# Performance work log

Hardware: AMD Instinct MI355X
Metric: run time of the kernel (lower is better)

Reference implementation:

```python
import jax, jax.numpy as jnp
import numpy as np

N, E, G = 10000, 80000, 32
Z, C, B, H = 10, 128, 8, 64
R_MAX = 5.0
AVG_NEIGH = 16.0
L_OFF = [0, 1, 4, 9, 16]  # slice offsets for l = 0..3 blocks of the SH vector


def real_sh(u):
    # Real spherical harmonics up to l=3, 'component' normalization (sum_m Y_lm^2 = 2l+1)
    x, y, z = u[:, 0], u[:, 1], u[:, 2]
    s3, s5, s15 = 3.0 ** 0.5, 5.0 ** 0.5, 15.0 ** 0.5
    cols = [
        jnp.ones_like(x),
        s3 * x, s3 * y, s3 * z,
        s15 * x * y, s15 * y * z, (s5 / 2) * (3 * z ** 2 - 1),
        s15 * x * z, (s15 / 2) * (x ** 2 - y ** 2),
        (70.0 ** 0.5 / 4) * (3 * x ** 2 * y - y ** 3),
        105.0 ** 0.5 * x * y * z,
        (42.0 ** 0.5 / 4) * y * (5 * z ** 2 - 1),
        (7.0 ** 0.5 / 2) * (5 * z ** 3 - 3 * z),
        (42.0 ** 0.5 / 4) * x * (5 * z ** 2 - 1),
        (105.0 ** 0.5 / 2) * z * (x ** 2 - y ** 2),
        (70.0 ** 0.5 / 4) * (x ** 3 - 3 * x * y ** 2),
    ]
    return jnp.stack(cols, axis=-1)  # [E, 16]


def poly_cutoff(x, p=5):
    f = (1.0 - (p + 1) * (p + 2) / 2 * x ** p
         + p * (p + 2) * x ** (p + 1)
         - p * (p + 1) / 2 * x ** (p + 2))
    return f * (x < 1.0).astype(f.dtype)


def setup_inputs() -> dict:
    key = jax.random.key(0)
    ks = jax.random.split(key, 20)
    vectors = jax.random.normal(ks[0], (E, 3), dtype=jnp.float32) * 1.5
    elem = jax.random.randint(ks[1], (N,), 0, Z)
    node_attrs = jax.nn.one_hot(elem, Z, dtype=jnp.float32)
    edge_index = jax.random.randint(ks[2], (2, E), 0, N).astype(jnp.int64)
    batch = jnp.sort(jax.random.randint(ks[3], (N,), 0, G)).astype(jnp.int64)

    def init(k, shape, fan_in):
        return jax.random.normal(k, shape, dtype=jnp.float32) / np.sqrt(fan_in)

    return {
        "vectors": vectors,
        "node_attrs": node_attrs,
        "W_embed": init(ks[4], (Z, C), Z),
        "atomic_energies": -jnp.arange(1, Z + 1, dtype=jnp.float32),
        "rw1": init(ks[5], (2, B, H), B),
        "rw2": init(ks[6], (2, H, H), H),
        "rw3": init(ks[7], (2, H, H), H),
        "rw4": init(ks[8], (2, H, 4 * C), H),
        "Wmix": init(ks[9], (2, 4, C, C), C),
        "U": init(ks[10], (2, Z, 4), Z),
        "Wprod": init(ks[11], (2, C, C), C),
        "Wsc": init(ks[12], (2, C, C), C),
        "Wro0": init(ks[13], (C, 1), C),
        "Wro1a": init(ks[14], (C, 16), C),
        "Wro1b": init(ks[15], (16, 1), 16),
        "scale": jnp.array([1.0], dtype=jnp.float32),
        "shift": jnp.array([0.0], dtype=jnp.float32),
        "edge_index": edge_index,
        "batch": batch,
    }


def reference(vectors, node_attrs, W_embed, atomic_energies, rw1, rw2, rw3, rw4,
              Wmix, U, Wprod, Wsc, Wro0, Wro1a, Wro1b, scale, shift,
              edge_index, batch):
    sender, receiver = edge_index[0], edge_index[1]
    r = jnp.linalg.norm(vectors, axis=-1)                     # [E]
    u = vectors / r[:, None]
    Y = real_sh(u)                                            # [E, 16]
    n = jnp.arange(1, B + 1, dtype=vectors.dtype)
    bessel = jnp.sqrt(2.0 / R_MAX) * jnp.sin(n[None] * jnp.pi * r[:, None] / R_MAX) / r[:, None]
    edge_feats = bessel * poly_cutoff(r / R_MAX)[:, None]     # [E, B]

    h = node_attrs @ W_embed                                  # [N, C] node embedding
    node_e0 = node_attrs @ atomic_energies                    # [N] atomic reference energies
    e0 = jax.ops.segment_sum(node_e0, batch, num_segments=G)  # [G]

    node_inter = jnp.zeros((node_attrs.shape[0],), dtype=vectors.dtype)
    for i in range(2):  # interaction layers (fixed small count)
        f = jax.nn.silu(edge_feats @ rw1[i])
        f = jax.nn.silu(f @ rw2[i])
        f = jax.nn.silu(f @ rw3[i])
        R_w = (f @ rw4[i]).reshape(-1, 4, C)                  # [E, 4, C] radial weights per l-path
        hs = h[sender]                                        # [E, C] edge gather
        A_parts = []
        for l in range(4):
            # channelwise tensor product (uvu): scalar node feats x Y_l -> l
            m = (R_w[:, l, :] * hs)[:, :, None] * Y[:, None, L_OFF[l]:L_OFF[l + 1]]  # [E, C, 2l+1]
            agg = jax.ops.segment_sum(m, receiver, num_segments=node_attrs.shape[0]) / AVG_NEIGH
            A_parts.append(jnp.einsum('ncm,cd->ndm', agg, Wmix[i, l]))
        # product basis: rotation-invariant powers per l, element-dependent contraction
        inv = jnp.stack([(p ** 2).sum(-1) for p in A_parts], axis=-1)  # [N, C, 4]
        w = node_attrs @ U[i]                                          # [N, 4]
        h = jnp.einsum('ncl,nl->nc', inv, w) @ Wprod[i] + h @ Wsc[i]   # product + residual sc
        if i == 0:
            node_inter = node_inter + (h @ Wro0)[:, 0]                 # linear readout
        else:
            node_inter = node_inter + (jax.nn.silu(h @ Wro1a) @ Wro1b)[:, 0]  # nonlinear readout
    node_inter = scale[0] * node_inter + shift[0]                       # scale-shift
    total = e0 + jax.ops.segment_sum(node_inter, batch, num_segments=G)
    return total  # [G] per-graph energies
```

## Files before the change

kernel.cpp:

```cpp
#include <hip/hip_runtime.h>

#define NN 10000
#define NE 80000
#define NG 32
#define NZ 10
#define NC 128
#define RMAXF 5.0f

typedef _Float16 f16;
typedef _Float16 half8 __attribute__((ext_vector_type(8)));
typedef float f32x4 __attribute__((ext_vector_type(4)));

__device__ __forceinline__ float silu_f(float x) {
    return x / (1.0f + __expf(-x));
}

__device__ __forceinline__ int clampi(int v, int lo, int hi) {
    return v < lo ? lo : (v > hi ? hi : v);
}

__device__ __forceinline__ uint4 pack8f(float4 a, float4 b) {
    union { f16 h[8]; uint4 u; } P;
    P.h[0] = (f16)a.x; P.h[1] = (f16)a.y; P.h[2] = (f16)a.z; P.h[3] = (f16)a.w;
    P.h[4] = (f16)b.x; P.h[5] = (f16)b.y; P.h[6] = (f16)b.z; P.h[7] = (f16)b.w;
    return P.u;
}

__global__ void zero_stuff(int* counts, int* cursor, float* out) {
    int i = blockIdx.x * blockDim.x + threadIdx.x;
    if (i < NN) { counts[i] = 0; cursor[i] = 0; }
    if (i < NG) out[i] = 0.0f;
}

__global__ void prep_weights(const float* __restrict__ Wmix, const float* __restrict__ Wprod,
                             const float* __restrict__ Wsc,
                             const float* __restrict__ rw2, const float* __restrict__ rw3,
                             const float* __restrict__ rw4,
                             f16* __restrict__ WmixT, f16* __restrict__ WprodT, f16* __restrict__ WscT,
                             f16* __restrict__ w2T, f16* __restrict__ w3T, f16* __restrict__ w4T) {
    int i = blockIdx.x * blockDim.x + threadIdx.x;
    if (i < 2 * 4 * 128 * 128) {
        int cc = i & 127, d = (i >> 7) & 127, g = i >> 14;
        WmixT[i] = (f16)Wmix[((size_t)g * 128 + cc) * 128 + d];
    }
    if (i < 2 * 128 * 128) {
        int cc = i & 127, d = (i >> 7) & 127, g = i >> 14;
        WprodT[i] = (f16)Wprod[((size_t)g * 128 + cc) * 128 + d];
        WscT[i]   = (f16)Wsc[((size_t)g * 128 + cc) * 128 + d];
    }
    if (i < 2 * 512 * 64) {
        int k = i & 63, j = (i >> 6) & 511, ly = i >> 15;
        w4T[i] = (f16)rw4[((size_t)ly * 64 + k) * 512 + j];
    }
    if (i < 2 * 64 * 64) {
        int k = i & 63, j = (i >> 6) & 63, ly = i >> 12;
        w2T[i] = (f16)rw2[((size_t)ly * 64 + k) * 64 + j];
        w3T[i] = (f16)rw3[((size_t)ly * 64 + k) * 64 + j];
    }
}

__global__ void node_init(const float* __restrict__ attrs, const float* __restrict__ W_embed,
                          const float* __restrict__ ae, const float* __restrict__ U,
                          float* __restrict__ h, float* __restrict__ node_e0, float* __restrict__ wU) {
    int gid = blockIdx.x * blockDim.x + threadIdx.x;
    if (gid >= NN * NC) return;
    int n = gid >> 7, c = gid & 127;
    float a[NZ];
#pragma unroll
    for (int z = 0; z < NZ; z++) a[z] = attrs[n * NZ + z];
    float acc = 0.f;
#pragma unroll
    for (int z = 0; z < NZ; z++) acc += a[z] * W_embed[z * NC + c];
    h[(size_t)n * NC + c] = acc;
    if (c == 0) {
        float e = 0.f;
#pragma unroll
        for (int z = 0; z < NZ; z++) e += a[z] * ae[z];
        node_e0[n] = e;
    }
    if (c < 8) {
        int i = c >> 2, l = c & 3;
        float s = 0.f;
#pragma unroll
        for (int z = 0; z < NZ; z++) s += a[z] * U[i * NZ * 4 + z * 4 + l];
        wU[(size_t)i * NN * 4 + n * 4 + l] = s;
    }
}

__global__ void edge_geom(const float* __restrict__ vec, float* __restrict__ Y, float* __restrict__ ef) {
    int e = blockIdx.x * blockDim.x + threadIdx.x;
    if (e >= NE) return;
    float vx = vec[e * 3 + 0], vy = vec[e * 3 + 1], vz = vec[e * 3 + 2];
    float r = sqrtf(vx * vx + vy * vy + vz * vz);
    float inv = 1.0f / r;
    float x = vx * inv, y = vy * inv, z = vz * inv;
    const float s3 = 1.7320508075688772f;
    const float s5 = 2.23606797749979f;
    const float s15 = 3.872983346207417f;
    const float c9 = 2.091650066335189f;
    const float c10 = 10.246950765959598f;
    const float c11 = 1.6201851746019651f;
    const float c12 = 1.3228756555322954f;
    const float c14 = 5.123475382979799f;
    float o[16];
    o[0] = 1.0f;
    o[1] = s3 * x; o[2] = s3 * y; o[3] = s3 * z;
    o[4] = s15 * x * y; o[5] = s15 * y * z; o[6] = 0.5f * s5 * (3.f * z * z - 1.f);
    o[7] = s15 * x * z; o[8] = 0.5f * s15 * (x * x - y * y);
    o[9] = c9 * (3.f * x * x * y - y * y * y);
    o[10] = c10 * x * y * z;
    o[11] = c11 * y * (5.f * z * z - 1.f);
    o[12] = c12 * (5.f * z * z * z - 3.f * z);
    o[13] = c11 * x * (5.f * z * z - 1.f);
    o[14] = c14 * z * (x * x - y * y);
    o[15] = c9 * (x * x * x - 3.f * x * y * y);
#pragma unroll
    for (int m = 0; m < 16; m++) Y[(size_t)e * 16 + m] = o[m];
    float xc = r / RMAXF;
    float cut = 0.0f;
    if (xc < 1.0f) {
        float x5 = xc * xc * xc * xc * xc;
        cut = 1.0f - 21.0f * x5 + 35.0f * x5 * xc - 15.0f * x5 * xc * xc;
    }
    float pref = sqrtf(2.0f / RMAXF) * inv * cut;
#pragma unroll
    for (int b = 0; b < 8; b++) {
        float arg = (float)(b + 1) * 3.14159265358979323846f * r / RMAXF;
        ef[(size_t)e * 8 + b] = pref * sinf(arg);
    }
}

__global__ void hist_recv(const int* __restrict__ recv, int* __restrict__ counts) {
    int e = blockIdx.x * blockDim.x + threadIdx.x;
    if (e < NE) atomicAdd(&counts[clampi(recv[e], 0, NN - 1)], 1);
}

__global__ void scan_counts(const int* __restrict__ counts, int* __restrict__ rowstart) {
    __shared__ int part[1024];
    int t = threadIdx.x;
    const int CH = 10;
    int base = t * CH;
    int loc[CH];
    int s = 0;
#pragma unroll
    for (int j = 0; j < CH; j++) {
        int v = (base + j < NN) ? counts[base + j] : 0;
        loc[j] = s; s += v;
    }
    part[t] = s;
    __syncthreads();
    for (int off = 1; off < 1024; off <<= 1) {
        int v = (t >= off) ? part[t - off] : 0;
        __syncthreads();
        part[t] += v;
        __syncthreads();
    }
    int chunk = (t > 0) ? part[t - 1] : 0;
#pragma unroll
    for (int j = 0; j < CH; j++)
        if (base + j < NN) rowstart[base + j] = chunk + loc[j];
    if (t == 0) rowstart[NN] = part[1023];
}

__global__ void scatter_edges(const int* __restrict__ recv, const int* __restrict__ rowstart,
                              int* __restrict__ cursor, int* __restrict__ elist) {
    int e = blockIdx.x * blockDim.x + threadIdx.x;
    if (e < NE) {
        int r = clampi(recv[e], 0, NN - 1);
        int p = atomicAdd(&cursor[r], 1);
        int slot = clampi(rowstart[r] + p, 0, NE - 1);
        elist[slot] = e;
    }
}

__global__ __launch_bounds__(256) void edge_mlp(const float* __restrict__ ef,
                                                const float* __restrict__ w1,
                                                const f16* __restrict__ w2T, const f16* __restrict__ w3T,
                                                const f16* __restrict__ w4T,
                                                f16* __restrict__ Rw) {
    __shared__ __align__(16) char L[16384];
    char* X1 = L;
    char* X2 = L + 8192;

    int tid = threadIdx.x;
    int lane = tid & 63;
    int w = tid >> 6;
    int ln = lane & 15, kq = lane >> 4;
    int eb = blockIdx.x * 64;

    {
        int jb = w * 16;
        const float4* efv = (const float4*)(ef + (size_t)(eb + lane) * 8);
        float4 ea = efv[0], eb4 = efv[1];
        float in8[8] = {ea.x, ea.y, ea.z, ea.w, eb4.x, eb4.y, eb4.z, eb4.w};
        f16 pk[16];
#pragma unroll
        for (int j = 0; j < 16; j++) {
            float a = 0.f;
#pragma unroll
            for (int b = 0; b < 8; b++) a += in8[b] * w1[b * 64 + jb + j];
            pk[j] = (f16)silu_f(a);
        }
        int base = lane * 128 + jb * 2;
#pragma unroll
        for (int t = 0; t < 2; t++) {
            int byte = (base + t * 16) ^ ((lane & 7) << 4);
            *(uint4*)(X1 + byte) = ((uint4*)pk)[t];
        }
    }
    __syncthreads();

    {
        half8 a[2];
#pragma unroll
        for (int kc = 0; kc < 2; kc++) {
            int row = w * 16 + ln;
            int byte = (row * 128 + kc * 64 + kq * 16) ^ ((row & 7) << 4);
            a[kc] = *(const half8*)(X1 + byte);
        }
#pragma unroll
        for (int nt = 0; nt < 4; nt++) {
            f32x4 acc = {0.f, 0.f, 0.f, 0.f};
#pragma unroll
            for (int kc = 0; kc < 2; kc++) {
                half8 b = *(const half8*)(w2T + (nt * 16 + ln) * 64 + kc * 32 + kq * 8);
                acc = __builtin_amdgcn_mfma_f32_16x16x32_f16(a[kc], b, acc, 0, 0, 0);
            }
#pragma unroll
            for (int r = 0; r < 4; r++) {
                int row = w * 16 + kq * 4 + r;
                int byte = (row * 128 + (nt * 16 + ln) * 2) ^ ((row & 7) << 4);
                *(f16*)(X2 + byte) = (f16)silu_f(acc[r]);
            }
        }
    }
    __syncthreads();

    {
        half8 a[2];
#pragma unroll
        for (int kc = 0; kc < 2; kc++) {
            int row = w * 16 + ln;
            int byte = (row * 128 + kc * 64 + kq * 16) ^ ((row & 7) << 4);
            a[kc] = *(const half8*)(X2 + byte);
        }
#pragma unroll
        for (int nt = 0; nt < 4; nt++) {
            f32x4 acc = {0.f, 0.f, 0.f, 0.f};
#pragma unroll
            for (int kc = 0; kc < 2; kc++) {
                half8 b = *(const half8*)(w3T + (nt * 16 + ln) * 64 + kc * 32 + kq * 8);
                acc = __builtin_amdgcn_mfma_f32_16x16x32_f16(a[kc], b, acc, 0, 0, 0);
            }
#pragma unroll
            for (int r = 0; r < 4; r++) {
                int row = w * 16 + kq * 4 + r;
                int byte = (row * 128 + (nt * 16 + ln) * 2) ^ ((row & 7) << 4);
                *(f16*)(X1 + byte) = (f16)silu_f(acc[r]);
            }
        }
    }
    __syncthreads();

    half8 a3[2];
#pragma unroll
    for (int kc = 0; kc < 2; kc++) {
        int row = w * 16 + ln;
        int byte = (row * 128 + kc * 64 + kq * 16) ^ ((row & 7) << 4);
        a3[kc] = *(const half8*)(X1 + byte);
    }
    for (int s = 0; s < 8; s++) {
#pragma unroll
        for (int nt = 0; nt < 4; nt++) {
            f32x4 acc = {0.f, 0.f, 0.f, 0.f};
#pragma unroll
            for (int kc = 0; kc < 2; kc++) {
                half8 b = *(const half8*)(w4T + (s * 64 + nt * 16 + ln) * 64 + kc * 32 + kq * 8);
                acc = __builtin_amdgcn_mfma_f32_16x16x32_f16(a3[kc], b, acc, 0, 0, 0);
            }
#pragma unroll
            for (int r = 0; r < 4; r++) {
                int row = w * 16 + kq * 4 + r;
                int byte = (row * 128 + (nt * 16 + ln) * 2) ^ ((row & 7) << 4);
                *(f16*)(X2 + byte) = (f16)acc[r];
            }
        }
        __syncthreads();
#pragma unroll
        for (int it = 0; it < 2; it++) {
            int i = it * 256 + tid;
            int row = i >> 3, chunk = i & 7;
            int byte = (row * 128 + chunk * 16) ^ ((row & 7) << 4);
            uint4 v = *(const uint4*)(X2 + byte);
            *(uint4*)(Rw + (size_t)(eb + row) * 512 + s * 64 + chunk * 8) = v;
        }
        __syncthreads();
    }
}

__global__ __launch_bounds__(256) void agg_only(const int* __restrict__ rowstart, const int* __restrict__ elist,
                                                const int* __restrict__ send, const float* __restrict__ h_in,
                                                const f16* __restrict__ Rw, const float* __restrict__ Y,
                                                f16* __restrict__ aggH) {
    __shared__ int eL[64], sL[64];
    int n = blockIdx.x, tid = threadIdx.x;
    int c = tid & 127, mh = tid >> 7;
    float acc[8];
#pragma unroll
    for (int q = 0; q < 8; q++) acc[q] = 0.f;
    int beg = rowstart[n], end = rowstart[n + 1];
    for (int base = beg; base < end; base += 64) {
        int cnt = min(64, end - base);
        __syncthreads();
        if (tid < cnt) {
            int e = clampi(elist[base + tid], 0, NE - 1);
            eL[tid] = e;
            sL[tid] = clampi(send[e], 0, NN - 1);
        }
        __syncthreads();
        for (int idx = 0; idx < cnt; idx++) {
            int e = eL[idx];
            int s = sL[idx];
            float hs = h_in[(size_t)s * NC + c];
            const f16* rwp = Rw + (size_t)e * 512;
            float y[8];
#pragma unroll
            for (int q = 0; q < 8; q++) y[q] = Y[(size_t)e * 16 + mh * 8 + q];
            if (mh == 0) {
                float p0 = (float)rwp[c] * hs;
                float p1 = (float)rwp[128 + c] * hs;
                float p2 = (float)rwp[256 + c] * hs;
                acc[0] += p0 * y[0];
                acc[1] += p1 * y[1]; acc[2] += p1 * y[2]; acc[3] += p1 * y[3];
                acc[4] += p2 * y[4]; acc[5] += p2 * y[5]; acc[6] += p2 * y[6]; acc[7] += p2 * y[7];
            } else {
                float p2 = (float)rwp[256 + c] * hs;
                float p3 = (float)rwp[384 + c] * hs;
                acc[0] += p2 * y[0];
#pragma unroll
                for (int q = 1; q < 8; q++) acc[q] += p3 * y[q];
            }
        }
    }
    const float inv16 = 1.0f / 16.0f;
#pragma unroll
    for (int q = 0; q < 8; q++)
        aggH[(size_t)n * 2048 + (size_t)(mh * 8 + q) * NC + c] = (f16)(acc[q] * inv16);
}

__global__ __launch_bounds__(512) void mix_mfma(
    const f16* __restrict__ aggH, const f16* __restrict__ WmixT,
    const float* __restrict__ wU, const float* __restrict__ h_in,
    const f16* __restrict__ WprodT, const f16* __restrict__ WscT,
    const float* __restrict__ Wro0, const float* __restrict__ Wro1a, const float* __restrict__ Wro1b,
    float* __restrict__ h_out, float* __restrict__ ni, int layer)
{
    __shared__ __align__(16) char Lb[32768];
    float* invwL = (float*)(Lb);
    f16*   invwH = (f16*)(Lb + 8192);
    f16*   hH    = (f16*)(Lb + 12288);
    f16*   houtH = (f16*)(Lb + 16384);
    float* p16L  = (float*)(Lb + 20480);

    int tid = threadIdx.x;
    int nb = blockIdx.x * 16;
    int lane = tid & 63;
    int w = tid >> 6;
    int ln = lane & 15, kq = lane >> 4;
    char* myB = Lb + w * 4096;

    float4 wUreg[4];
#pragma unroll
    for (int r = 0; r < 4; r++)
        wUreg[r] = *(const float4*)(wU + (size_t)(nb + kq * 4 + r) * 4);

    float invwacc[4] = {0.f, 0.f, 0.f, 0.f};
    const f16* aggRow = aggH + (size_t)(nb + ln) * 2048 + kq * 8;

#pragma unroll
    for (int g = 0; g < 4; g++) {
        const int mstart = (g == 0) ? 0 : (g == 1) ? 1 : (g == 2) ? 4 : 9;
        const int mend   = (g == 0) ? 1 : (g == 1) ? 4 : (g == 2) ? 9 : 16;
        {
            const f16* Bt = WmixT + ((size_t)(layer * 4 + g) << 14);
#pragma unroll
            for (int i = 0; i < 4; i++) {
                int q = i * 64 + lane;
                int row = q >> 4, col = q & 15;
                uint4 v = *(const uint4*)(Bt + (w * 16 + row) * 128 + col * 8);
                int byte = (row * 256 + col * 16) ^ ((row & 7) << 4);
                *(uint4*)(myB + byte) = v;
            }
        }
#pragma unroll
        for (int m = mstart; m < mend; m++) {
            f32x4 acc = {0.f, 0.f, 0.f, 0.f};
#pragma unroll
            for (int k = 0; k < 4; k++) {
                half8 a = *(const half8*)(aggRow + m * 128 + k * 32);
                int byte = (ln * 256 + k * 64 + kq * 16) ^ ((ln & 7) << 4);
                half8 b = *(const half8*)(myB + byte);
                acc = __builtin_amdgcn_mfma_f32_16x16x32_f16(a, b, acc, 0, 0, 0);
            }
#pragma unroll
            for (int r = 0; r < 4; r++) {
                float wur = (g == 0) ? wUreg[r].x : (g == 1) ? wUreg[r].y : (g == 2) ? wUreg[r].z : wUreg[r].w;
                invwacc[r] += acc[r] * acc[r] * wur;
            }
        }
    }
    __syncthreads();

#pragma unroll
    for (int r = 0; r < 4; r++)
        invwL[(kq * 4 + r) * 128 + w * 16 + ln] = invwacc[r];
    __syncthreads();

    if (tid < 256) {
        int node = tid >> 4, ch = tid & 15;
        int byte = (node * 256 + ch * 16) ^ ((node & 7) << 4);
        float4 v0 = *(float4*)&invwL[node * 128 + ch * 8];
        float4 v1 = *(float4*)&invwL[node * 128 + ch * 8 + 4];
        *(uint4*)((char*)invwH + byte) = pack8f(v0, v1);
        const float4* hp = (const float4*)(h_in + (size_t)(nb + node) * 128 + ch * 8);
        float4 g0 = hp[0], g1 = hp[1];
        *(uint4*)((char*)hH + byte) = pack8f(g0, g1);
    }
    __syncthreads();

    {
        half8 ai[4], ah[4];
#pragma unroll
        for (int k = 0; k < 4; k++) {
            int byte = (ln * 256 + (k * 32 + kq * 8) * 2) ^ ((ln & 7) << 4);
            ai[k] = *(const half8*)((char*)invwH + byte);
            ah[k] = *(const half8*)((char*)hH + byte);
        }
        const f16* Bp = WprodT + ((size_t)layer << 14);
        const f16* Bs = WscT + ((size_t)layer << 14);
        f32x4 acc = {0.f, 0.f, 0.f, 0.f};
#pragma unroll
        for (int k = 0; k < 4; k++) {
            half8 bb = *(const half8*)(Bp + (w * 16 + ln) * 128 + k * 32 + kq * 8);
            acc = __builtin_amdgcn_mfma_f32_16x16x32_f16(ai[k], bb, acc, 0, 0, 0);
        }
#pragma unroll
        for (int k = 0; k < 4; k++) {
            half8 bb = *(const half8*)(Bs + (w * 16 + ln) * 128 + k * 32 + kq * 8);
            acc = __builtin_amdgcn_mfma_f32_16x16x32_f16(ah[k], bb, acc, 0, 0, 0);
        }
#pragma unroll
        for (int r = 0; r < 4; r++) {
            int node = kq * 4 + r;
            int d = w * 16 + ln;
            h_out[(size_t)(nb + node) * 128 + d] = acc[r];
            houtH[node * 128 + d] = (f16)acc[r];
        }
    }
    __syncthreads();

    if (tid < 256) {
        int rn = tid >> 4, rj = tid & 15;
        if (layer == 0) {
            float s = 0.f;
            for (int cc = rj; cc < 128; cc += 16) s += (float)houtH[rn * 128 + cc] * Wro0[cc];
            p16L[tid] = s;
        } else {
            float s = 0.f;
            for (int cc = 0; cc < 128; cc++) s += (float)houtH[rn * 128 + cc] * Wro1a[cc * 16 + rj];
            s = silu_f(s);
            p16L[tid] = s * Wro1b[rj];
        }
    }
    __syncthreads();
    if (tid < 16) {
        float t = 0.f;
#pragma unroll
        for (int j = 0; j < 16; j++) t += p16L[tid * 16 + j];
        ni[nb + tid] = (layer == 0) ? t : (ni[nb + tid] + t);
    }
}

__global__ void finalize(const float* __restrict__ node_e0, const float* __restrict__ ni,
                         const int* __restrict__ batch, const float* __restrict__ scale,
                         const float* __restrict__ shift, float* __restrict__ out) {
    __shared__ float bins[NG];
    int tid = threadIdx.x;
    if (tid < NG) bins[tid] = 0.f;
    __syncthreads();
    int n = blockIdx.x * blockDim.x + tid;
    if (n < NN) {
        float v = node_e0[n] + scale[0] * ni[n] + shift[0];
        atomicAdd(&bins[clampi(batch[n], 0, NG - 1)], v);
    }
    __syncthreads();
    if (tid < NG) atomicAdd(&out[tid], bins[tid]);
}

extern "C" void kernel_launch(void* const* d_in, const int* in_sizes, int n_in,
                              void* d_out, int out_size, void* d_ws, size_t ws_size,
                              hipStream_t stream) {
    (void)in_sizes; (void)n_in; (void)out_size; (void)ws_size;
    const float* vectors = (const float*)d_in[0];
    const float* attrs   = (const float*)d_in[1];
    const float* W_embed = (const float*)d_in[2];
    const float* ae      = (const float*)d_in[3];
    const float* rw1     = (const float*)d_in[4];
    const float* rw2     = (const float*)d_in[5];
    const float* rw3     = (const float*)d_in[6];
    const float* rw4     = (const float*)d_in[7];
    const float* Wmix    = (const float*)d_in[8];
    const float* U       = (const float*)d_in[9];
    const float* Wprod   = (const float*)d_in[10];
    const float* Wsc     = (const float*)d_in[11];
    const float* Wro0    = (const float*)d_in[12];
    const float* Wro1a   = (const float*)d_in[13];
    const float* Wro1b   = (const float*)d_in[14];
    const float* scale   = (const float*)d_in[15];
    const float* shift   = (const float*)d_in[16];
    const int* eidx      = (const int*)d_in[17];
    const int* batch     = (const int*)d_in[18];
    float* out = (float*)d_out;

    char* w = (char*)d_ws;
    size_t off = 0;
    auto alloc = [&](size_t bytes) -> void* {
        void* p = (void*)(w + off);
        off += (bytes + 255) & ~(size_t)255;
        return p;
    };
    float* Y       = (float*)alloc((size_t)NE * 16 * 4);
    float* ef      = (float*)alloc((size_t)NE * 8 * 4);
    f16*   Rw      = (f16*)  alloc((size_t)NE * 512 * 2);
    f16*   aggH    = (f16*)  alloc((size_t)NN * 2048 * 2);
    float* hA      = (float*)alloc((size_t)NN * NC * 4);
    float* hB      = (float*)alloc((size_t)NN * NC * 4);
    float* wU      = (float*)alloc((size_t)2 * NN * 4 * 4);
    float* node_e0 = (float*)alloc((size_t)NN * 4);
    float* ni      = (float*)alloc((size_t)NN * 4);
    f16*   WmixT   = (f16*)  alloc((size_t)2 * 4 * 128 * 128 * 2);
    f16*   WprodT  = (f16*)  alloc((size_t)2 * 128 * 128 * 2);
    f16*   WscT    = (f16*)  alloc((size_t)2 * 128 * 128 * 2);
    f16*   w2T     = (f16*)  alloc((size_t)2 * 64 * 64 * 2);
    f16*   w3T     = (f16*)  alloc((size_t)2 * 64 * 64 * 2);
    f16*   w4T     = (f16*)  alloc((size_t)2 * 512 * 64 * 2);
    int* counts    = (int*)alloc((size_t)NN * 4);
    int* rowstart  = (int*)alloc((size_t)(NN + 1) * 4);
    int* cursor    = (int*)alloc((size_t)NN * 4);
    int* elist     = (int*)alloc((size_t)NE * 4);

    const int* send = eidx;
    const int* recv = eidx + NE;
    zero_stuff<<<(NN + 255) / 256, 256, 0, stream>>>(counts, cursor, out);
    prep_weights<<<512, 256, 0, stream>>>(Wmix, Wprod, Wsc, rw2, rw3, rw4,
                                          WmixT, WprodT, WscT, w2T, w3T, w4T);
    node_init<<<(NN * NC + 255) / 256, 256, 0, stream>>>(attrs, W_embed, ae, U, hA, node_e0, wU);
    edge_geom<<<(NE + 255) / 256, 256, 0, stream>>>(vectors, Y, ef);
    hist_recv<<<(NE + 255) / 256, 256, 0, stream>>>(recv, counts);
    scan_counts<<<1, 1024, 0, stream>>>(counts, rowstart);
    scatter_edges<<<(NE + 255) / 256, 256, 0, stream>>>(recv, rowstart, cursor, elist);

    float* hcur = hA;
    float* hnext = hB;
    for (int layer = 0; layer < 2; layer++) {
        edge_mlp<<<NE / 64, 256, 0, stream>>>(
            ef, rw1 + layer * 8 * 64,
            w2T + (size_t)layer * 64 * 64, w3T + (size_t)layer * 64 * 64,
            w4T + (size_t)layer * 512 * 64, Rw);
        agg_only<<<NN, 256, 0, stream>>>(rowstart, elist, send, hcur, Rw, Y, aggH);
        mix_mfma<<<NN / 16, 512, 0, stream>>>(
            aggH, WmixT, wU + (size_t)layer * NN * 4, hcur,
            WprodT, WscT, Wro0, Wro1a, Wro1b, hnext, ni, layer);
        float* t = hcur; hcur = hnext; hnext = t;
    }
    finalize<<<(NN + 255) / 256, 256, 0, stream>>>(node_e0, ni, batch, scale, shift, out);
}
```

Baseline: 349.0 us.

## Split mix kernel into per-half Wmix stage and product/readout stage

The fused mix kernel is split in two. The first kernel computes the Wmix projections and invariant contraction, using two 256-thread blocks per 16-node tile, each covering half the output channels. It writes fp16 results to a new global buffer. The second kernel reads that buffer for the Wprod/Wsc matmuls and the readout. The aim is more blocks and lower LDS per block for better occupancy, at the cost of an extra launch and a global round trip for the intermediate.

Result: faster. 337.7 us (-3.2%).

```diff
diff --git a/kernel.cpp b/kernel.cpp
--- a/kernel.cpp
+++ b/kernel.cpp
@@ -348,80 +348,91 @@
         aggH[(size_t)n * 2048 + (size_t)(mh * 8 + q) * NC + c] = (f16)(acc[q] * inv16);
 }
 
-__global__ __launch_bounds__(512) void mix_mfma(
+__global__ __launch_bounds__(256) void mix_a(
     const f16* __restrict__ aggH, const f16* __restrict__ WmixT,
-    const float* __restrict__ wU, const float* __restrict__ h_in,
+    const float* __restrict__ wU, f16* __restrict__ invwG, int layer)
+{
+    __shared__ __align__(16) char Lb[16384];
+
+    int tid = threadIdx.x;
+    int b = blockIdx.x;
+    int nb = (b >> 1) * 16;
+    int half = b & 1;
+    int lane = tid & 63;
+    int w = tid >> 6;
+    int dt = half * 4 + w;
+    int ln = lane & 15, kq = lane >> 4;
+    char* myB = Lb + w * 4096;
+
+    float4 wUreg[4];
+#pragma unroll
+    for (int r = 0; r < 4; r++)
+        wUreg[r] = *(const float4*)(wU + (size_t)(nb + kq * 4 + r) * 4);
+
+    float invwacc[4] = {0.f, 0.f, 0.f, 0.f};
+    const f16* aggRow = aggH + (size_t)(nb + ln) * 2048 + kq * 8;
+
+#pragma unroll
+    for (int g = 0; g < 4; g++) {
+        const int mstart = (g == 0) ? 0 : (g == 1) ? 1 : (g == 2) ? 4 : 9;
+        const int mend   = (g == 0) ? 1 : (g == 1) ? 4 : (g == 2) ? 9 : 16;
+        {
+            const f16* Bt = WmixT + ((size_t)(layer * 4 + g) << 14);
+#pragma unroll
+            for (int i = 0; i < 4; i++) {
+                int q = i * 64 + lane;
+                int row = q >> 4, col = q & 15;
+                uint4 v = *(const uint4*)(Bt + (dt * 16 + row) * 128 + col * 8);
+                int byte = (row * 256 + col * 16) ^ ((row & 7) << 4);
+                *(uint4*)(myB + byte) = v;
+            }
+        }
+#pragma unroll
+        for (int m = mstart; m < mend; m++) {
+            f32x4 acc = {0.f, 0.f, 0.f, 0.f};
+#pragma unroll
+            for (int k = 0; k < 4; k++) {
+                half8 a = *(const half8*)(aggRow + m * 128 + k * 32);
+                int byte = (ln * 256 + k * 64 + kq * 16) ^ ((ln & 7) << 4);
+                half8 bb = *(const half8*)(myB + byte);
+                acc = __builtin_amdgcn_mfma_f32_16x16x32_f16(a, bb, acc, 0, 0, 0);
+            }
+#pragma unroll
+            for (int r = 0; r < 4; r++) {
+                float wur = (g == 0) ? wUreg[r].x : (g == 1) ? wUreg[r].y : (g == 2) ? wUreg[r].z : wUreg[r].w;
+                invwacc[r] += acc[r] * acc[r] * wur;
+            }
+        }
+    }
+
+#pragma unroll
+    for (int r = 0; r < 4; r++)
+        invwG[(size_t)(nb + kq * 4 + r) * 128 + dt * 16 + ln] = (f16)invwacc[r];
+}
+
+__global__ __launch_bounds__(512) void mix_b(
+    const f16* __restrict__ invwG, const float* __restrict__ h_in,
     const f16* __restrict__ WprodT, const f16* __restrict__ WscT,
     const float* __restrict__ Wro0, const float* __restrict__ Wro1a, const float* __restrict__ Wro1b,
     float* __restrict__ h_out, float* __restrict__ ni, int layer)
 {
-    __shared__ __align__(16) char Lb[32768];
-    float* invwL = (float*)(Lb);
-    f16*   invwH = (f16*)(Lb + 8192);
-    f16*   hH    = (f16*)(Lb + 12288);
-    f16*   houtH = (f16*)(Lb + 16384);
-    float* p16L  = (float*)(Lb + 20480);
+    __shared__ __align__(16) char Lb[13312];
+    f16*   invwH = (f16*)(Lb);
+    f16*   hH    = (f16*)(Lb + 4096);
+    f16*   houtH = (f16*)(Lb + 8192);
+    float* p16L  = (float*)(Lb + 12288);
 
     int tid = threadIdx.x;
     int nb = blockIdx.x * 16;
     int lane = tid & 63;
     int w = tid >> 6;
     int ln = lane & 15, kq = lane >> 4;
-    char* myB = Lb + w * 4096;
-
-    float4 wUreg[4];
-#pragma unroll
-    for (int r = 0; r < 4; r++)
-        wUreg[r] = *(const float4*)(wU + (size_t)(nb + kq * 4 + r) * 4);
-
-    float invwacc[4] = {0.f, 0.f, 0.f, 0.f};
-    const f16* aggRow = aggH + (size_t)(nb + ln) * 2048 + kq * 8;
-
-#pragma unroll
-    for (int g = 0; g < 4; g++) {
-        const int mstart = (g == 0) ? 0 : (g == 1) ? 1 : (g == 2) ? 4 : 9;
-        const int mend   = (g == 0) ? 1 : (g == 1) ? 4 : (g == 2) ? 9 : 16;
-        {
-            const f16* Bt = WmixT + ((size_t)(layer * 4 + g) << 14);
-#pragma unroll
-            for (int i = 0; i < 4; i++) {
-                int q = i * 64 + lane;
-                int row = q >> 4, col = q & 15;
-                uint4 v = *(const uint4*)(Bt + (w * 16 + row) * 128 + col * 8);
-                int byte = (row * 256 + col * 16) ^ ((row & 7) << 4);
-                *(uint4*)(myB + byte) = v;
-            }
-        }
-#pragma unroll
-        for (int m = mstart; m < mend; m++) {
-            f32x4 acc = {0.f, 0.f, 0.f, 0.f};
-#pragma unroll
-            for (int k = 0; k < 4; k++) {
-                half8 a = *(const half8*)(aggRow + m * 128 + k * 32);
-                int byte = (ln * 256 + k * 64 + kq * 16) ^ ((ln & 7) << 4);
-                half8 b = *(const half8*)(myB + byte);
-                acc = __builtin_amdgcn_mfma_f32_16x16x32_f16(a, b, acc, 0, 0, 0);
-            }
-#pragma unroll
-            for (int r = 0; r < 4; r++) {
-                float wur = (g == 0) ? wUreg[r].x : (g == 1) ? wUreg[r].y : (g == 2) ? wUreg[r].z : wUreg[r].w;
-                invwacc[r] += acc[r] * acc[r] * wur;
-            }
-        }
-    }
-    __syncthreads();
-
-#pragma unroll
-    for (int r = 0; r < 4; r++)
-        invwL[(kq * 4 + r) * 128 + w * 16 + ln] = invwacc[r];
-    __syncthreads();
 
     if (tid < 256) {
         int node = tid >> 4, ch = tid & 15;
         int byte = (node * 256 + ch * 16) ^ ((node & 7) << 4);
-        float4 v0 = *(float4*)&invwL[node * 128 + ch * 8];
-        float4 v1 = *(float4*)&invwL[node * 128 + ch * 8 + 4];
-        *(uint4*)((char*)invwH + byte) = pack8f(v0, v1);
+        uint4 iv = *(const uint4*)(invwG + (size_t)(nb + node) * 128 + ch * 8);
+        *(uint4*)((char*)invwH + byte) = iv;
         const float4* hp = (const float4*)(h_in + (size_t)(nb + node) * 128 + ch * 8);
         float4 g0 = hp[0], g1 = hp[1];
         *(uint4*)((char*)hH + byte) = pack8f(g0, g1);
@@ -535,6 +546,7 @@
     f16*   aggH    = (f16*)  alloc((size_t)NN * 2048 * 2);
     float* hA      = (float*)alloc((size_t)NN * NC * 4);
     float* hB      = (float*)alloc((size_t)NN * NC * 4);
+    f16*   invwG   = (f16*)  alloc((size_t)NN * NC * 2);
     float* wU      = (float*)alloc((size_t)2 * NN * 4 * 4);
     float* node_e0 = (float*)alloc((size_t)NN * 4);
     float* ni      = (float*)alloc((size_t)NN * 4);
@@ -568,9 +580,10 @@
             w2T + (size_t)layer * 64 * 64, w3T + (size_t)layer * 64 * 64,
             w4T + (size_t)layer * 512 * 64, Rw);
         agg_only<<<NN, 256, 0, stream>>>(rowstart, elist, send, hcur, Rw, Y, aggH);
-        mix_mfma<<<NN / 16, 512, 0, stream>>>(
-            aggH, WmixT, wU + (size_t)layer * NN * 4, hcur,
-            WprodT, WscT, Wro0, Wro1a, Wro1b, hnext, ni, layer);
+        mix_a<<<(NN / 16) * 2, 256, 0, stream>>>(
+            aggH, WmixT, wU + (size_t)layer * NN * 4, invwG, layer);
+        mix_b<<<NN / 16, 512, 0, stream>>>(
+            invwG, hcur, WprodT, WscT, Wro0, Wro1a, Wro1b, hnext, ni, layer);
         float* t = hcur; hcur = hnext; hnext = t;
     }
     finalize<<<(NN + 255) / 256, 256, 0, stream>>>(node_e0, ni, batch, scale, shift, out);
```
